# Optimization experiments

Measured on AMD Instinct MI355X. Metric: run time of the kernel, lower is better.

The kernel has to match this reference:

```python
import jax, jax.numpy as jnp
import numpy as np


def _lecun_tanh(x):
    return 1.7159 * jnp.tanh(0.666 * x)


def _lin_init(k, fan_in, fan_out):
    s = 1.0 / np.sqrt(fan_in)
    kw, kb = jax.random.split(k)
    W = jax.random.uniform(kw, (fan_in, fan_out), minval=-s, maxval=s, dtype=jnp.float32)
    b = jax.random.uniform(kb, (fan_out,), minval=-s, maxval=s, dtype=jnp.float32)
    return W, b


def setup_inputs() -> dict:
    key = jax.random.key(0)
    ks = jax.random.split(key, 8)
    B, T, OBS, H, A = 256, 1024, 32, 128, 8
    Wb, bb = _lin_init(ks[0], OBS + H, H)      # backbone Linear
    Wff1, bff1 = _lin_init(ks[1], H, H)
    Wff2, bff2 = _lin_init(ks[2], H, H)
    Wta, bta = _lin_init(ks[3], H, H)          # time_a
    Wtb, btb = _lin_init(ks[4], H, H)          # time_b
    Wa, ba = _lin_init(ks[5], H, A)            # actor head
    Wc, bc = _lin_init(ks[6], H, 1)            # critic head
    obs = jax.random.normal(ks[7], (B, T, OBS), dtype=jnp.float32)
    return dict(obs=obs, Wb=Wb, bb=bb, Wff1=Wff1, bff1=bff1, Wff2=Wff2, bff2=bff2,
                Wta=Wta, bta=bta, Wtb=Wtb, btb=btb, Wa=Wa, ba=ba, Wc=Wc, bc=bc)


def reference(obs, Wb, bb, Wff1, bff1, Wff2, bff2, Wta, bta, Wtb, btb, Wa, ba, Wc, bc):
    # CfCActorCritic.forward_sequence: CfC (default mode, 1 backbone layer, ts=1)
    # scanned over time, then actor/critic heads on every timestep output.
    B, T, _ = obs.shape
    H = Wff1.shape[0]
    ts = 1.0

    def step(h, x_t):
        z = jnp.concatenate([x_t, h], axis=-1)          # [B, OBS+H]
        z = _lecun_tanh(z @ Wb + bb)                    # backbone MLP
        ff1 = jnp.tanh(z @ Wff1 + bff1)
        ff2 = jnp.tanh(z @ Wff2 + bff2)
        t_interp = jax.nn.sigmoid((z @ Wta + bta) * ts + (z @ Wtb + btb))
        h_new = ff1 * (1.0 - t_interp) + t_interp * ff2
        return h_new, h_new

    h0 = jnp.zeros((B, H), dtype=obs.dtype)
    obs_t = jnp.swapaxes(obs, 0, 1)                     # [T, B, OBS]
    _, ys = jax.lax.scan(step, h0, obs_t)               # ys: [T, B, H]
    out = jnp.swapaxes(ys, 0, 1)                        # [B, T, H]
    mean = out @ Wa + ba                                # [B, T, A]
    value = (out @ Wc + bc).squeeze(-1)                 # [B, T]
    return mean, value
```

## Files before the change

### kernel.cpp

```cpp
#include <hip/hip_runtime.h>


typedef _Float16 half8 __attribute__((ext_vector_type(8)));
typedef float f32x4 __attribute__((ext_vector_type(4)));

#define T_STEPS 1024
#define OBS 32
#define H 128
#define A_DIM 8
#define NW 8
#define NT (NW * 64)
#define ROWS 4
#define NBLK 64

#define ZIN_P 164
#define ZF_P 132

__device__ __forceinline__ float fexp2(float x) { return __builtin_amdgcn_exp2f(x); }
__device__ __forceinline__ float frcp(float x) { return __builtin_amdgcn_rcpf(x); }

__device__ __forceinline__ void sync_lds() {
    __builtin_amdgcn_sched_barrier(0);
    asm volatile("s_waitcnt lgkmcnt(0)" ::: "memory");
    __builtin_amdgcn_s_barrier();
    __builtin_amdgcn_sched_barrier(0);
}

__global__ void __launch_bounds__(NT) cfc_kernel(
    const float* __restrict__ obs,
    const float* __restrict__ Wb,  const float* __restrict__ bb,
    const float* __restrict__ Wff1, const float* __restrict__ bff1,
    const float* __restrict__ Wff2, const float* __restrict__ bff2,
    const float* __restrict__ Wta, const float* __restrict__ bta,
    const float* __restrict__ Wtb, const float* __restrict__ btb,
    const float* __restrict__ Wa,  const float* __restrict__ ba,
    const float* __restrict__ Wc,  const float* __restrict__ bc,
    float* __restrict__ out_mean, float* __restrict__ out_value)
{
    const int b0 = blockIdx.x * ROWS;
    const int tid = threadIdx.x;
    const int w = tid >> 6, l = tid & 63;
    const int lo = l & 15, hi = l >> 4;

    __shared__ _Float16 zin[16][ZIN_P];
    __shared__ _Float16 zf[16][ZF_P];

    const int colB = w * 16 + lo;

    half8 Bb[5];
#pragma unroll
    for (int ks = 0; ks < 5; ++ks)
#pragma unroll
        for (int j = 0; j < 8; ++j) {
            int k = ks * 32 + hi * 8 + j;
            Bb[ks][j] = (_Float16)Wb[k * H + colB];
        }
    const float bbv = bb[colB];

    half8 Bg0[4], Bg1[4], Bg2[4];
#pragma unroll
    for (int ks = 0; ks < 4; ++ks)
#pragma unroll
        for (int j = 0; j < 8; ++j) {
            int k = ks * 32 + hi * 8 + j;
            Bg0[ks][j] = (_Float16)Wff1[k * H + colB];
            Bg1[ks][j] = (_Float16)Wff2[k * H + colB];
            Bg2[ks][j] = (_Float16)(Wta[k * H + colB] + Wtb[k * H + colB]);
        }
    const float bg1 = bff1[colB], bg2 = bff2[colB], bg3 = bta[colB] + btb[colB];

    half8 Bh[4];
    float bh = 0.f;
    if (w == 7) {
#pragma unroll
        for (int ks = 0; ks < 4; ++ks)
#pragma unroll
            for (int j = 0; j < 8; ++j) {
                int k = ks * 32 + hi * 8 + j;
                float v = (lo < 8) ? Wa[k * A_DIM + lo] : ((lo == 8) ? Wc[k] : 0.0f);
                Bh[ks][j] = (_Float16)v;
            }
        bh = (lo < 8) ? ba[lo] : ((lo == 8) ? bc[0] : 0.0f);
    }

    for (int i = tid; i < 16 * ZIN_P; i += NT) (&zin[0][0])[i] = (_Float16)0.0f;
    __syncthreads();
    const int rX = (w << 1) | (l >> 5), cX = l & 31;
    if (w < 2) zin[rX][cX] = (_Float16)obs[((size_t)(b0 + rX) * T_STEPS) * OBS + cX];
    __syncthreads();

    float oxA = 0.f, oxB = 0.f;
    if (w < 2) {
        oxA = obs[((size_t)(b0 + rX) * T_STEPS + 1) * OBS + cX];
        oxB = obs[((size_t)(b0 + rX) * T_STEPS + 2) * OBS + cX];
    }

    for (int t = 0; t < T_STEPS; ++t) {
        half8 A0 = *(const half8*)&zin[lo][0 * 32 + hi * 8];
        half8 A1 = *(const half8*)&zin[lo][1 * 32 + hi * 8];
        half8 A2 = *(const half8*)&zin[lo][2 * 32 + hi * 8];
        half8 A3 = *(const half8*)&zin[lo][3 * 32 + hi * 8];
        half8 A4 = *(const half8*)&zin[lo][4 * 32 + hi * 8];
        f32x4 az0 = {bbv, bbv, bbv, bbv};
        f32x4 az1 = {0.f, 0.f, 0.f, 0.f};
        az0 = __builtin_amdgcn_mfma_f32_16x16x32_f16(A0, Bb[0], az0, 0, 0, 0);
        az1 = __builtin_amdgcn_mfma_f32_16x16x32_f16(A1, Bb[1], az1, 0, 0, 0);
        az0 = __builtin_amdgcn_mfma_f32_16x16x32_f16(A2, Bb[2], az0, 0, 0, 0);
        az1 = __builtin_amdgcn_mfma_f32_16x16x32_f16(A3, Bb[3], az1, 0, 0, 0);
        az0 = __builtin_amdgcn_mfma_f32_16x16x32_f16(A4, Bb[4], az0, 0, 0, 0);

        if (w == 7 && t > 0) {
            f32x4 acch = {bh, bh, bh, bh};
            acch = __builtin_amdgcn_mfma_f32_16x16x32_f16(A1, Bh[0], acch, 0, 0, 0);
            acch = __builtin_amdgcn_mfma_f32_16x16x32_f16(A2, Bh[1], acch, 0, 0, 0);
            acch = __builtin_amdgcn_mfma_f32_16x16x32_f16(A3, Bh[2], acch, 0, 0, 0);
            acch = __builtin_amdgcn_mfma_f32_16x16x32_f16(A4, Bh[3], acch, 0, 0, 0);
            if (hi == 0 && lo < 9) {
#pragma unroll
                for (int j = 0; j < 4; ++j) {
                    if (lo < 8) out_mean[((size_t)(b0 + j) * T_STEPS + (t - 1)) * A_DIM + lo] = acch[j];
                    else        out_value[(size_t)(b0 + j) * T_STEPS + (t - 1)] = acch[j];
                }
            }
        }

#pragma unroll
        for (int j = 0; j < 4; ++j) {
            float s = az0[j] + az1[j];
            float r = frcp(fexp2(1.9216697f * s) + 1.0f);
            zf[hi * 4 + j][colB] = (_Float16)fmaf(-3.4318f, r, 1.7159f);
        }
        sync_lds();

        half8 Z0 = *(const half8*)&zf[lo][0 * 32 + hi * 8];
        half8 Z1 = *(const half8*)&zf[lo][1 * 32 + hi * 8];
        half8 Z2 = *(const half8*)&zf[lo][2 * 32 + hi * 8];
        half8 Z3 = *(const half8*)&zf[lo][3 * 32 + hi * 8];
        f32x4 a1 = {bg1, bg1, bg1, bg1};
        f32x4 a2 = {bg2, bg2, bg2, bg2};
        f32x4 a3 = {bg3, bg3, bg3, bg3};
        a1 = __builtin_amdgcn_mfma_f32_16x16x32_f16(Z0, Bg0[0], a1, 0, 0, 0);
        a2 = __builtin_amdgcn_mfma_f32_16x16x32_f16(Z0, Bg1[0], a2, 0, 0, 0);
        a3 = __builtin_amdgcn_mfma_f32_16x16x32_f16(Z0, Bg2[0], a3, 0, 0, 0);
        a1 = __builtin_amdgcn_mfma_f32_16x16x32_f16(Z1, Bg0[1], a1, 0, 0, 0);
        a2 = __builtin_amdgcn_mfma_f32_16x16x32_f16(Z1, Bg1[1], a2, 0, 0, 0);
        a3 = __builtin_amdgcn_mfma_f32_16x16x32_f16(Z1, Bg2[1], a3, 0, 0, 0);
        a1 = __builtin_amdgcn_mfma_f32_16x16x32_f16(Z2, Bg0[2], a1, 0, 0, 0);
        a2 = __builtin_amdgcn_mfma_f32_16x16x32_f16(Z2, Bg1[2], a2, 0, 0, 0);
        a3 = __builtin_amdgcn_mfma_f32_16x16x32_f16(Z2, Bg2[2], a3, 0, 0, 0);
        a1 = __builtin_amdgcn_mfma_f32_16x16x32_f16(Z3, Bg0[3], a1, 0, 0, 0);
        a2 = __builtin_amdgcn_mfma_f32_16x16x32_f16(Z3, Bg1[3], a2, 0, 0, 0);
        a3 = __builtin_amdgcn_mfma_f32_16x16x32_f16(Z3, Bg2[3], a3, 0, 0, 0);

#pragma unroll
        for (int j = 0; j < 4; ++j) {
            float r1 = frcp(fexp2(2.8853901f * a1[j]) + 1.0f);
            float ff1 = fmaf(-2.0f, r1, 1.0f);
            float r2 = frcp(fexp2(2.8853901f * a2[j]) + 1.0f);
            float ff2 = fmaf(-2.0f, r2, 1.0f);
            float ti = frcp(1.0f + fexp2(-1.44269504f * a3[j]));
            zin[hi * 4 + j][32 + colB] = (_Float16)(ff1 + ti * (ff2 - ff1));
        }

        if (w < 2 && t + 1 < T_STEPS) {
            zin[rX][cX] = (_Float16)oxA;
            oxA = oxB;
            const int tf = t + 3;
            oxB = (tf < T_STEPS) ? obs[((size_t)(b0 + rX) * T_STEPS + tf) * OBS + cX] : 0.0f;
        }
        sync_lds();
    }

    if (w == 7) {
        half8 A1 = *(const half8*)&zin[lo][32 + 0 * 32 + hi * 8];
        half8 A2 = *(const half8*)&zin[lo][32 + 1 * 32 + hi * 8];
        half8 A3 = *(const half8*)&zin[lo][32 + 2 * 32 + hi * 8];
        half8 A4 = *(const half8*)&zin[lo][32 + 3 * 32 + hi * 8];
        f32x4 acch = {bh, bh, bh, bh};
        acch = __builtin_amdgcn_mfma_f32_16x16x32_f16(A1, Bh[0], acch, 0, 0, 0);
        acch = __builtin_amdgcn_mfma_f32_16x16x32_f16(A2, Bh[1], acch, 0, 0, 0);
        acch = __builtin_amdgcn_mfma_f32_16x16x32_f16(A3, Bh[2], acch, 0, 0, 0);
        acch = __builtin_amdgcn_mfma_f32_16x16x32_f16(A4, Bh[3], acch, 0, 0, 0);
        if (hi == 0 && lo < 9) {
#pragma unroll
            for (int j = 0; j < 4; ++j) {
                if (lo < 8) out_mean[((size_t)(b0 + j) * T_STEPS + (T_STEPS - 1)) * A_DIM + lo] = acch[j];
                else        out_value[(size_t)(b0 + j) * T_STEPS + (T_STEPS - 1)] = acch[j];
            }
        }
    }
}

extern "C" void kernel_launch(void* const* d_in, const int* in_sizes, int n_in,
                              void* d_out, int out_size, void* d_ws, size_t ws_size,
                              hipStream_t stream) {
    (void)in_sizes; (void)n_in; (void)d_ws; (void)ws_size; (void)out_size;
    const float* obs  = (const float*)d_in[0];
    const float* Wb   = (const float*)d_in[1];
    const float* bb   = (const float*)d_in[2];
    const float* Wff1 = (const float*)d_in[3];
    const float* bff1 = (const float*)d_in[4];
    const float* Wff2 = (const float*)d_in[5];
    const float* bff2 = (const float*)d_in[6];
    const float* Wta  = (const float*)d_in[7];
    const float* bta  = (const float*)d_in[8];
    const float* Wtb  = (const float*)d_in[9];
    const float* btb  = (const float*)d_in[10];
    const float* Wa   = (const float*)d_in[11];
    const float* ba   = (const float*)d_in[12];
    const float* Wc   = (const float*)d_in[13];
    const float* bc   = (const float*)d_in[14];
    float* out = (float*)d_out;
    float* out_mean  = out;
    float* out_value = out + (size_t)256 * 1024 * 8;

    cfc_kernel<<<dim3(NBLK), dim3(NT), 0, stream>>>(
        obs, Wb, bb, Wff1, bff1, Wff2, bff2, Wta, bta, Wtb, btb,
        Wa, ba, Wc, bc, out_mean, out_value);
}
```

Measured before the change: 1.137 ms.

## Defer actor/critic head to post-scan pass via fp16 hidden-state history in workspace

Removes the per-timestep actor/critic head MFMAs and scattered output stores from warp 7 inside the serial recurrence. Each hidden state is instead written as fp16 to a workspace buffer, and after the scan all warps compute the heads for every timestep in a batched loop. This shortens the latency-critical recurrent step. The cost is extra global writes and reads of a 64MB history buffer, and the path depends on the workspace being large enough, otherwise it falls back to the old kernel.

```diff
diff --git a/kernel.cpp b/kernel.cpp
--- a/kernel.cpp
+++ b/kernel.cpp
@@ -26,6 +26,7 @@
     __builtin_amdgcn_sched_barrier(0);
 }
 
+template<bool OFFLOAD>
 __global__ void __launch_bounds__(NT) cfc_kernel(
     const float* __restrict__ obs,
     const float* __restrict__ Wb,  const float* __restrict__ bb,
@@ -35,7 +36,8 @@
     const float* __restrict__ Wtb, const float* __restrict__ btb,
     const float* __restrict__ Wa,  const float* __restrict__ ba,
     const float* __restrict__ Wc,  const float* __restrict__ bc,
-    float* __restrict__ out_mean, float* __restrict__ out_value)
+    float* __restrict__ out_mean, float* __restrict__ out_value,
+    _Float16* __restrict__ hist)
 {
     const int b0 = blockIdx.x * ROWS;
     const int tid = threadIdx.x;
@@ -71,7 +73,7 @@
 
     half8 Bh[4];
     float bh = 0.f;
-    if (w == 7) {
+    if (!OFFLOAD && w == 7) {
 #pragma unroll
         for (int ks = 0; ks < 4; ++ks)
 #pragma unroll
@@ -109,7 +111,7 @@
         az1 = __builtin_amdgcn_mfma_f32_16x16x32_f16(A3, Bb[3], az1, 0, 0, 0);
         az0 = __builtin_amdgcn_mfma_f32_16x16x32_f16(A4, Bb[4], az0, 0, 0, 0);
 
-        if (w == 7 && t > 0) {
+        if (!OFFLOAD && w == 7 && t > 0) {
             f32x4 acch = {bh, bh, bh, bh};
             acch = __builtin_amdgcn_mfma_f32_16x16x32_f16(A1, Bh[0], acch, 0, 0, 0);
             acch = __builtin_amdgcn_mfma_f32_16x16x32_f16(A2, Bh[1], acch, 0, 0, 0);
@@ -159,7 +161,10 @@
             float r2 = frcp(fexp2(2.8853901f * a2[j]) + 1.0f);
             float ff2 = fmaf(-2.0f, r2, 1.0f);
             float ti = frcp(1.0f + fexp2(-1.44269504f * a3[j]));
-            zin[hi * 4 + j][32 + colB] = (_Float16)(ff1 + ti * (ff2 - ff1));
+            _Float16 hv = (_Float16)(ff1 + ti * (ff2 - ff1));
+            zin[hi * 4 + j][32 + colB] = hv;
+            if (OFFLOAD && hi == 0)
+                hist[((size_t)(b0 + j) * T_STEPS + t) * H + colB] = hv;
         }
 
         if (w < 2 && t + 1 < T_STEPS) {
@@ -171,21 +176,58 @@
         sync_lds();
     }
 
-    if (w == 7) {
-        half8 A1 = *(const half8*)&zin[lo][32 + 0 * 32 + hi * 8];
-        half8 A2 = *(const half8*)&zin[lo][32 + 1 * 32 + hi * 8];
-        half8 A3 = *(const half8*)&zin[lo][32 + 2 * 32 + hi * 8];
-        half8 A4 = *(const half8*)&zin[lo][32 + 3 * 32 + hi * 8];
-        f32x4 acch = {bh, bh, bh, bh};
-        acch = __builtin_amdgcn_mfma_f32_16x16x32_f16(A1, Bh[0], acch, 0, 0, 0);
-        acch = __builtin_amdgcn_mfma_f32_16x16x32_f16(A2, Bh[1], acch, 0, 0, 0);
-        acch = __builtin_amdgcn_mfma_f32_16x16x32_f16(A3, Bh[2], acch, 0, 0, 0);
-        acch = __builtin_amdgcn_mfma_f32_16x16x32_f16(A4, Bh[3], acch, 0, 0, 0);
-        if (hi == 0 && lo < 9) {
-#pragma unroll
-            for (int j = 0; j < 4; ++j) {
-                if (lo < 8) out_mean[((size_t)(b0 + j) * T_STEPS + (T_STEPS - 1)) * A_DIM + lo] = acch[j];
-                else        out_value[(size_t)(b0 + j) * T_STEPS + (T_STEPS - 1)] = acch[j];
+    if (OFFLOAD) {
+        __syncthreads();
+        half8 Bh2[4];
+#pragma unroll
+        for (int ks = 0; ks < 4; ++ks)
+#pragma unroll
+            for (int j = 0; j < 8; ++j) {
+                int k = ks * 32 + hi * 8 + j;
+                float v = (lo < 8) ? Wa[k * A_DIM + lo] : ((lo == 8) ? Wc[k] : 0.0f);
+                Bh2[ks][j] = (_Float16)v;
+            }
+        const float bh2 = (lo < 8) ? ba[lo] : ((lo == 8) ? bc[0] : 0.0f);
+
+        for (int c = w; c < 256; c += NW) {
+            const int r = c >> 6;
+            const int s0 = (c & 63) << 4;
+            const _Float16* hp = hist + ((size_t)(b0 + r) * T_STEPS + (s0 + lo)) * H + hi * 8;
+            half8 A0 = *(const half8*)(hp);
+            half8 A1 = *(const half8*)(hp + 32);
+            half8 A2 = *(const half8*)(hp + 64);
+            half8 A3 = *(const half8*)(hp + 96);
+            f32x4 acc = {bh2, bh2, bh2, bh2};
+            acc = __builtin_amdgcn_mfma_f32_16x16x32_f16(A0, Bh2[0], acc, 0, 0, 0);
+            acc = __builtin_amdgcn_mfma_f32_16x16x32_f16(A1, Bh2[1], acc, 0, 0, 0);
+            acc = __builtin_amdgcn_mfma_f32_16x16x32_f16(A2, Bh2[2], acc, 0, 0, 0);
+            acc = __builtin_amdgcn_mfma_f32_16x16x32_f16(A3, Bh2[3], acc, 0, 0, 0);
+            if (lo < 9) {
+#pragma unroll
+                for (int j = 0; j < 4; ++j) {
+                    const int s_ = s0 + hi * 4 + j;
+                    if (lo < 8) out_mean[((size_t)(b0 + r) * T_STEPS + s_) * A_DIM + lo] = acc[j];
+                    else        out_value[(size_t)(b0 + r) * T_STEPS + s_] = acc[j];
+                }
+            }
+        }
+    } else {
+        if (w == 7) {
+            half8 A1 = *(const half8*)&zin[lo][32 + 0 * 32 + hi * 8];
+            half8 A2 = *(const half8*)&zin[lo][32 + 1 * 32 + hi * 8];
+            half8 A3 = *(const half8*)&zin[lo][32 + 2 * 32 + hi * 8];
+            half8 A4 = *(const half8*)&zin[lo][32 + 3 * 32 + hi * 8];
+            f32x4 acch = {bh, bh, bh, bh};
+            acch = __builtin_amdgcn_mfma_f32_16x16x32_f16(A1, Bh[0], acch, 0, 0, 0);
+            acch = __builtin_amdgcn_mfma_f32_16x16x32_f16(A2, Bh[1], acch, 0, 0, 0);
+            acch = __builtin_amdgcn_mfma_f32_16x16x32_f16(A3, Bh[2], acch, 0, 0, 0);
+            acch = __builtin_amdgcn_mfma_f32_16x16x32_f16(A4, Bh[3], acch, 0, 0, 0);
+            if (hi == 0 && lo < 9) {
+#pragma unroll
+                for (int j = 0; j < 4; ++j) {
+                    if (lo < 8) out_mean[((size_t)(b0 + j) * T_STEPS + (T_STEPS - 1)) * A_DIM + lo] = acch[j];
+                    else        out_value[(size_t)(b0 + j) * T_STEPS + (T_STEPS - 1)] = acch[j];
+                }
             }
         }
     }
@@ -194,7 +236,7 @@
 extern "C" void kernel_launch(void* const* d_in, const int* in_sizes, int n_in,
                               void* d_out, int out_size, void* d_ws, size_t ws_size,
                               hipStream_t stream) {
-    (void)in_sizes; (void)n_in; (void)d_ws; (void)ws_size; (void)out_size;
+    (void)in_sizes; (void)n_in; (void)out_size;
     const float* obs  = (const float*)d_in[0];
     const float* Wb   = (const float*)d_in[1];
     const float* bb   = (const float*)d_in[2];
@@ -214,7 +256,14 @@
     float* out_mean  = out;
     float* out_value = out + (size_t)256 * 1024 * 8;
 
-    cfc_kernel<<<dim3(NBLK), dim3(NT), 0, stream>>>(
-        obs, Wb, bb, Wff1, bff1, Wff2, bff2, Wta, bta, Wtb, btb,
-        Wa, ba, Wc, bc, out_mean, out_value);
+    const size_t need = (size_t)256 * 1024 * 128 * sizeof(_Float16);
+    if (ws_size >= need) {
+        cfc_kernel<true><<<dim3(NBLK), dim3(NT), 0, stream>>>(
+            obs, Wb, bb, Wff1, bff1, Wff2, bff2, Wta, bta, Wtb, btb,
+            Wa, ba, Wc, bc, out_mean, out_value, (_Float16*)d_ws);
+    } else {
+        cfc_kernel<false><<<dim3(NBLK), dim3(NT), 0, stream>>>(
+            obs, Wb, bb, Wff1, bff1, Wff2, bff2, Wta, bta, Wtb, btb,
+            Wa, ba, Wc, bc, out_mean, out_value, (_Float16*)d_ws);
+    }
 }
```

New measurement: 1.082 ms. 4.8% less time.
